# Kernel tuning notes

Measured on AMD Instinct MI355X. Metric: run time of the kernel, lower is better.

The kernel has to match this reference:

```python
import jax, jax.numpy as jnp
import numpy as np

H = 1024      # hidden_size
I = 512       # moe_intermediate_size
E = 8         # n_routed_experts
K = 2         # num_experts_per_tok
SI = I * 2    # shared expert intermediate (n_shared_experts=2)
B, S = 2, 1024


def setup_inputs() -> dict:
    key = jax.random.key(0)
    ks = jax.random.split(key, 9)
    s = 0.02
    return {
        "x": jax.random.normal(ks[0], (B, S, H), jnp.float32),
        "gate_w": jax.random.normal(ks[1], (E, H), jnp.float32) * s,
        "lb_bias": jnp.zeros((E,), jnp.float32),
        "expert_gate_w": jax.random.normal(ks[2], (E, I, H), jnp.float32) * s,
        "expert_up_w": jax.random.normal(ks[3], (E, I, H), jnp.float32) * s,
        "expert_down_w": jax.random.normal(ks[4], (E, H, I), jnp.float32) * s,
        "shared_gate_w": jax.random.normal(ks[5], (SI, H), jnp.float32) * s,
        "shared_up_w": jax.random.normal(ks[6], (SI, H), jnp.float32) * s,
        "shared_down_w": jax.random.normal(ks[7], (H, SI), jnp.float32) * s,
    }


def _mlp(x, gw, uw, dw):
    # SwiGLU: down( silu(gate(x)) * up(x) )
    return (jax.nn.silu(x @ gw.T) * (x @ uw.T)) @ dw.T


def reference(x, gate_w, lb_bias, expert_gate_w, expert_up_w, expert_down_w,
              shared_gate_w, shared_up_w, shared_down_w):
    b, s, h = x.shape
    xf = x.reshape(-1, h)                                   # [T, H]
    # --- SimpleRouter (sigmoid scoring) ---
    logits = xf @ gate_w.T + lb_bias                        # [T, E]
    scores = jax.nn.sigmoid(logits.astype(jnp.float32))
    topw, topi = jax.lax.top_k(scores, K)                   # [T, K]
    topw = (topw / (topw.sum(-1, keepdims=True) + 1e-8)).astype(x.dtype)
    # --- _process_local: per-expert dispatch/compute/combine ---
    # Faithful to torch source: expert_weights[mask].mean(dim=-1) collapses to a
    # SCALAR per expert (mean routing weight over all tokens sent to that expert).
    out = jnp.zeros_like(xf)
    for e in range(E):
        m = (topi == e)                                     # [T, K]
        sel = m.any(axis=-1)                                # [T]
        cnt = m.sum()
        wmean = (topw * m).sum() / jnp.maximum(cnt, 1).astype(topw.dtype)
        y = _mlp(xf, expert_gate_w[e], expert_up_w[e], expert_down_w[e])  # [T, H]
        out = out + jnp.where(sel[:, None], y * wmean, jnp.zeros((), x.dtype))
    out = out.reshape(b, s, h)
    # --- shared experts ---
    out = out + _mlp(x, shared_gate_w, shared_up_w, shared_down_w)
    return out
```

## Files before the change

### kernel.cpp

```cpp
#include <hip/hip_runtime.h>

#define H_DIM 1024
#define I_DIM 512
#define NE 8
#define SI_DIM 1024
#define NT 2048
#define NS 4096

typedef __bf16 bf16;
typedef __bf16 bf16x4 __attribute__((ext_vector_type(4)));
typedef __bf16 bf16x8 __attribute__((ext_vector_type(8)));
typedef float f32x4 __attribute__((ext_vector_type(4)));

#define W_EG 0
#define W_EU (NE * I_DIM * H_DIM)
#define W_ED (2 * NE * I_DIM * H_DIM)
#define W_SG (3 * NE * I_DIM * H_DIM)
#define W_SU (W_SG + SI_DIM * H_DIM)
#define W_SD (W_SU + SI_DIM * H_DIM)
#define W_TOT (W_SD + H_DIM * SI_DIM)

#define OFF_CNT 0
#define OFF_WM 64
#define OFF_BASE 128
#define OFF_TOPI 1024
#define OFF_TOPW (OFF_TOPI + NT * 8)
#define OFF_GSLOT (OFF_TOPW + NT * 8)
#define OFF_LISTS (OFF_GSLOT + NT * 8)
#define OFF_WB (OFF_LISTS + NS * 4)
#define OFF_XB (OFF_WB + W_TOT * 2)
#define OFF_XG (OFF_XB + NT * H_DIM * 2)
#define OFF_ACTE (OFF_XG + (NS + 128) * H_DIM * 2)
#define OFF_ACTS (OFF_ACTE + (NS + 128) * I_DIM * 2)
#define OFF_YDE (OFF_ACTS + (size_t)NT * SI_DIM * 2)
#define OFF_YDS (OFF_YDE + (size_t)NS * H_DIM * 2)

__device__ __forceinline__ bf16x4 cvt4(f32x4 v) {
  bf16x4 r;
  r.x = (bf16)v.x; r.y = (bf16)v.y; r.z = (bf16)v.z; r.w = (bf16)v.w;
  return r;
}

__device__ __forceinline__ void glds16(const bf16* g, bf16* l) {
  __builtin_amdgcn_global_load_lds(
      (const __attribute__((address_space(1))) unsigned int*)g,
      (__attribute__((address_space(3))) unsigned int*)l, 16, 0, 0);
}

__global__ __launch_bounds__(256) void convert_w(
    const float* __restrict__ eg, const float* __restrict__ eu,
    const float* __restrict__ ed, const float* __restrict__ sg,
    const float* __restrict__ su, const float* __restrict__ sd,
    bf16* __restrict__ wb) {
  size_t i = ((size_t)blockIdx.x * 256 + threadIdx.x) * 4;
  if (i >= W_TOT) return;
  const float* src;
  size_t o;
  if (i < W_EU)      { src = eg; o = i - W_EG; }
  else if (i < W_ED) { src = eu; o = i - W_EU; }
  else if (i < W_SG) { src = ed; o = i - W_ED; }
  else if (i < W_SU) { src = sg; o = i - W_SG; }
  else if (i < W_SD) { src = su; o = i - W_SU; }
  else               { src = sd; o = i - W_SD; }
  *(bf16x4*)(wb + i) = cvt4(*(const f32x4*)(src + o));
}

__global__ __launch_bounds__(256) void router_kernel(
    const float* __restrict__ x, const float* __restrict__ gw,
    const float* __restrict__ lb, int2* __restrict__ topi,
    float2* __restrict__ topw) {
  const int lane = threadIdx.x & 63;
  const int t = blockIdx.x * 4 + (threadIdx.x >> 6);
  const float* xr = x + (size_t)t * H_DIM;

  float s[NE];
#pragma unroll
  for (int e = 0; e < NE; e++) s[e] = 0.f;
#pragma unroll
  for (int k0 = 0; k0 < H_DIM; k0 += 256) {
    f32x4 xv = *(const f32x4*)(xr + k0 + lane * 4);
#pragma unroll
    for (int e = 0; e < NE; e++) {
      f32x4 gv = *(const f32x4*)(gw + e * H_DIM + k0 + lane * 4);
      s[e] += xv.x * gv.x + xv.y * gv.y + xv.z * gv.z + xv.w * gv.w;
    }
  }
#pragma unroll
  for (int e = 0; e < NE; e++) {
    float v = s[e];
#pragma unroll
    for (int off = 32; off > 0; off >>= 1) v += __shfl_xor(v, off);
    s[e] = v;
  }
  if (lane == 0) {
    float sc[NE];
#pragma unroll
    for (int e = 0; e < NE; e++) sc[e] = 1.f / (1.f + expf(-(s[e] + lb[e])));
    int i1 = 0;
#pragma unroll
    for (int e = 1; e < NE; e++)
      if (sc[e] > sc[i1]) i1 = e;
    int i2 = -1;
#pragma unroll
    for (int e = 0; e < NE; e++) {
      if (e == i1) continue;
      if (i2 < 0 || sc[e] > sc[i2]) i2 = e;
    }
    float w1 = sc[i1], w2 = sc[i2];
    float inv = 1.f / (w1 + w2 + 1e-8f);
    topi[t] = make_int2(i1, i2);
    topw[t] = make_float2(w1 * inv, w2 * inv);
  }
}

__global__ __launch_bounds__(512) void build_kernel(
    const int2* __restrict__ topi, const float2* __restrict__ topw,
    int* __restrict__ cnt, float* __restrict__ wm, int* __restrict__ base,
    int* __restrict__ lists, int2* __restrict__ gslot) {
  __shared__ int cnt_l[NE];
  __shared__ int base_l[NE + 1];
  const int e = threadIdx.x >> 6;
  const int lane = threadIdx.x & 63;

  int c = 0;
  float wacc = 0.f;
  for (int t0 = 0; t0 < NT; t0 += 64) {
    int2 ti = topi[t0 + lane];
    float2 tw = topw[t0 + lane];
    bool hit = (ti.x == e) || (ti.y == e);
    float w = (ti.x == e) ? tw.x : ((ti.y == e) ? tw.y : 0.f);
    c += __popcll(__ballot(hit));
#pragma unroll
    for (int off = 32; off > 0; off >>= 1) w += __shfl_xor(w, off);
    wacc += w;
  }
  if (lane == 0) {
    cnt_l[e] = c;
    cnt[e] = c;
    wm[e] = wacc / (float)(c > 0 ? c : 1);
  }
  __syncthreads();
  if (threadIdx.x == 0) {
    int b = 0;
    for (int i = 0; i < NE; i++) {
      base_l[i] = b;
      base[i] = b;
      b += cnt_l[i];
    }
    base_l[NE] = b;
    base[NE] = b;
  }
  __syncthreads();

  int pos = base_l[e];
  for (int t0 = 0; t0 < NT; t0 += 64) {
    int t = t0 + lane;
    int2 ti = topi[t];
    bool hit = (ti.x == e) || (ti.y == e);
    unsigned long long m = __ballot(hit);
    int pre = __popcll(m & ((1ull << lane) - 1ull));
    if (hit) {
      int g = pos + pre;
      lists[g] = t;
      if (ti.x == e) gslot[t].x = g;
      else gslot[t].y = g;
    }
    pos += __popcll(m);
  }
}

__global__ __launch_bounds__(256) void gather_kernel(
    const float* __restrict__ x, const int* __restrict__ lists,
    bf16* __restrict__ xg, bf16* __restrict__ xb) {
  int b = blockIdx.x;
  const float* src;
  bf16* dst;
  if (b < NS) {
    src = x + (size_t)lists[b] * H_DIM;
    dst = xg + (size_t)b * H_DIM;
  } else {
    int r = b - NS;
    src = x + (size_t)r * H_DIM;
    dst = xb + (size_t)r * H_DIM;
  }
  int c = threadIdx.x * 4;
  *(bf16x4*)(dst + c) = cvt4(*(const f32x4*)(src + c));
}

__global__ __launch_bounds__(256, 2) void gemm_gu(
    const bf16* __restrict__ wb, const bf16* __restrict__ xg,
    const bf16* __restrict__ xb, const int* __restrict__ cnt,
    const int* __restrict__ base, bf16* __restrict__ act_e,
    bf16* __restrict__ act_s) {
  const int z = blockIdx.z, colTile = blockIdx.x, rowTile = blockIdx.y;
  const bf16 *Ab, *Gb, *Ub;
  bf16* Cp;
  int ldc, mrem;
  if (z < NE) {
    if (colTile >= I_DIM / 128) return;
    int c = cnt[z];
    if (rowTile * 128 >= c) return;
    int rb = base[z] + rowTile * 128;
    Ab = xg + (size_t)rb * H_DIM;
    Gb = wb + W_EG + (size_t)z * I_DIM * H_DIM + (size_t)colTile * 128 * H_DIM;
    Ub = wb + W_EU + (size_t)z * I_DIM * H_DIM + (size_t)colTile * 128 * H_DIM;
    Cp = act_e + (size_t)rb * I_DIM + colTile * 128;
    ldc = I_DIM;
    mrem = c - rowTile * 128;
  } else {
    Ab = xb + (size_t)rowTile * 128 * H_DIM;
    Gb = wb + W_SG + (size_t)colTile * 128 * H_DIM;
    Ub = wb + W_SU + (size_t)colTile * 128 * H_DIM;
    Cp = act_s + (size_t)rowTile * 128 * SI_DIM + colTile * 128;
    ldc = SI_DIM;
    mrem = 128;
  }

  __shared__ __align__(16) bf16 As[128 * 64];
  __shared__ __align__(16) bf16 Bgs[128 * 64];
  __shared__ __align__(16) bf16 Bus[128 * 64];

  const int tid = threadIdx.x;
  const int lane = tid & 63, wave = tid >> 6;
  const int mw = (wave >> 1) * 64, nw = (wave & 1) * 64;
  const int l15 = lane & 15, quad = lane >> 4;
  const int srow = tid >> 3;
  const int scol = (tid & 7) * 8;

  f32x4 ag[4][4] = {};
  f32x4 au[4][4] = {};

  for (int k0 = 0; k0 < H_DIM; k0 += 64) {
#pragma unroll
    for (int r = 0; r < 4; r++) {
      int row = srow + r * 32;
      glds16(Ab + (size_t)row * H_DIM + k0 + scol, &As[row * 64 + scol]);
    }
#pragma unroll
    for (int r = 0; r < 4; r++) {
      int row = srow + r * 32;
      glds16(Gb + (size_t)row * H_DIM + k0 + scol, &Bgs[row * 64 + scol]);
    }
#pragma unroll
    for (int r = 0; r < 4; r++) {
      int row = srow + r * 32;
      glds16(Ub + (size_t)row * H_DIM + k0 + scol, &Bus[row * 64 + scol]);
    }
    __syncthreads();
#pragma unroll
    for (int kk = 0; kk < 2; kk++) {
      const int kof = kk * 32 + quad * 8;
      bf16x8 av[4], gv[4], uv[4];
#pragma unroll
      for (int i = 0; i < 4; i++) {
        av[i] = *(const bf16x8*)&As[(mw + i * 16 + l15) * 64 + kof];
        gv[i] = *(const bf16x8*)&Bgs[(nw + i * 16 + l15) * 64 + kof];
        uv[i] = *(const bf16x8*)&Bus[(nw + i * 16 + l15) * 64 + kof];
      }
#pragma unroll
      for (int i = 0; i < 4; i++)
#pragma unroll
        for (int j = 0; j < 4; j++) {
          ag[i][j] = __builtin_amdgcn_mfma_f32_16x16x32_bf16(av[i], gv[j], ag[i][j], 0, 0, 0);
          au[i][j] = __builtin_amdgcn_mfma_f32_16x16x32_bf16(av[i], uv[j], au[i][j], 0, 0, 0);
        }
    }
    __syncthreads();
  }

#pragma unroll
  for (int i = 0; i < 4; i++) {
#pragma unroll
    for (int rg = 0; rg < 4; rg++) {
      int rl = mw + i * 16 + quad * 4 + rg;
      if (rl < mrem) {
#pragma unroll
        for (int j = 0; j < 4; j++) {
          int c = nw + j * 16 + l15;
          float g = ag[i][j][rg], u = au[i][j][rg];
          Cp[(size_t)rl * ldc + c] = (bf16)((g / (1.f + __expf(-g))) * u);
        }
      }
    }
  }
}

__global__ __launch_bounds__(256, 2) void gemm_down(
    const bf16* __restrict__ wb, const bf16* __restrict__ act_e,
    const bf16* __restrict__ act_s, const int* __restrict__ cnt,
    const int* __restrict__ base, bf16* __restrict__ yd_e,
    bf16* __restrict__ yd_s) {
  const int z = blockIdx.z, colTile = blockIdx.x, rowTile = blockIdx.y;
  const bf16 *Ab, *Bb;
  bf16* Cp;
  int K, mrem;
  if (z < NE) {
    int c = cnt[z];
    if (rowTile * 128 >= c) return;
    int rb = base[z] + rowTile * 128;
    Ab = act_e + (size_t)rb * I_DIM;
    K = I_DIM;
    Bb = wb + W_ED + (size_t)z * H_DIM * I_DIM + (size_t)colTile * 128 * I_DIM;
    Cp = yd_e + (size_t)rb * H_DIM + colTile * 128;
    mrem = c - rowTile * 128;
  } else {
    Ab = act_s + (size_t)rowTile * 128 * SI_DIM;
    K = SI_DIM;
    Bb = wb + W_SD + (size_t)colTile * 128 * SI_DIM;
    Cp = yd_s + (size_t)rowTile * 128 * H_DIM + colTile * 128;
    mrem = 128;
  }

  __shared__ __align__(16) bf16 As[128 * 64];
  __shared__ __align__(16) bf16 Bs[128 * 64];

  const int tid = threadIdx.x;
  const int lane = tid & 63, wave = tid >> 6;
  const int mw = (wave >> 1) * 64, nw = (wave & 1) * 64;
  const int l15 = lane & 15, quad = lane >> 4;
  const int srow = tid >> 3;
  const int scol = (tid & 7) * 8;

  f32x4 acc[4][4] = {};

  for (int k0 = 0; k0 < K; k0 += 64) {
#pragma unroll
    for (int r = 0; r < 4; r++) {
      int row = srow + r * 32;
      glds16(Ab + (size_t)row * K + k0 + scol, &As[row * 64 + scol]);
    }
#pragma unroll
    for (int r = 0; r < 4; r++) {
      int row = srow + r * 32;
      glds16(Bb + (size_t)row * K + k0 + scol, &Bs[row * 64 + scol]);
    }
    __syncthreads();
#pragma unroll
    for (int kk = 0; kk < 2; kk++) {
      const int kof = kk * 32 + quad * 8;
      bf16x8 av[4], bv[4];
#pragma unroll
      for (int i = 0; i < 4; i++) {
        av[i] = *(const bf16x8*)&As[(mw + i * 16 + l15) * 64 + kof];
        bv[i] = *(const bf16x8*)&Bs[(nw + i * 16 + l15) * 64 + kof];
      }
#pragma unroll
      for (int i = 0; i < 4; i++)
#pragma unroll
        for (int j = 0; j < 4; j++)
          acc[i][j] = __builtin_amdgcn_mfma_f32_16x16x32_bf16(av[i], bv[j], acc[i][j], 0, 0, 0);
    }
    __syncthreads();
  }

#pragma unroll
  for (int i = 0; i < 4; i++) {
#pragma unroll
    for (int rg = 0; rg < 4; rg++) {
      int rl = mw + i * 16 + quad * 4 + rg;
      if (rl < mrem) {
#pragma unroll
        for (int j = 0; j < 4; j++) {
          int c = nw + j * 16 + l15;
          Cp[(size_t)rl * H_DIM + c] = (bf16)acc[i][j][rg];
        }
      }
    }
  }
}

__global__ __launch_bounds__(256) void combine_kernel(
    const bf16* __restrict__ yd_e, const bf16* __restrict__ yd_s,
    const int2* __restrict__ topi, const int2* __restrict__ gslot,
    const float* __restrict__ wm, float* __restrict__ out) {
  int t = blockIdx.x;
  int2 ei = topi[t];
  int2 gi = gslot[t];
  float w1 = wm[ei.x], w2 = wm[ei.y];
  int c = threadIdx.x * 4;
  bf16x4 y1 = *(const bf16x4*)(yd_e + (size_t)gi.x * H_DIM + c);
  bf16x4 y2 = *(const bf16x4*)(yd_e + (size_t)gi.y * H_DIM + c);
  bf16x4 ys = *(const bf16x4*)(yd_s + (size_t)t * H_DIM + c);
  f32x4 o;
  o.x = w1 * (float)y1.x + w2 * (float)y2.x + (float)ys.x;
  o.y = w1 * (float)y1.y + w2 * (float)y2.y + (float)ys.y;
  o.z = w1 * (float)y1.z + w2 * (float)y2.z + (float)ys.z;
  o.w = w1 * (float)y1.w + w2 * (float)y2.w + (float)ys.w;
  *(f32x4*)(out + (size_t)t * H_DIM + c) = o;
}

extern "C" void kernel_launch(void* const* d_in, const int* in_sizes, int n_in,
                              void* d_out, int out_size, void* d_ws,
                              size_t ws_size, hipStream_t stream) {
  (void)in_sizes; (void)n_in; (void)out_size; (void)ws_size;
  const float* x  = (const float*)d_in[0];
  const float* gw = (const float*)d_in[1];
  const float* lb = (const float*)d_in[2];
  const float* eg = (const float*)d_in[3];
  const float* eu = (const float*)d_in[4];
  const float* ed = (const float*)d_in[5];
  const float* sg = (const float*)d_in[6];
  const float* su = (const float*)d_in[7];
  const float* sd = (const float*)d_in[8];
  float* out = (float*)d_out;
  char* ws = (char*)d_ws;

  int* cnt     = (int*)(ws + OFF_CNT);
  float* wm    = (float*)(ws + OFF_WM);
  int* base    = (int*)(ws + OFF_BASE);
  int2* topi   = (int2*)(ws + OFF_TOPI);
  float2* topw = (float2*)(ws + OFF_TOPW);
  int2* gslot  = (int2*)(ws + OFF_GSLOT);
  int* lists   = (int*)(ws + OFF_LISTS);
  bf16* wb     = (bf16*)(ws + OFF_WB);
  bf16* xb     = (bf16*)(ws + OFF_XB);
  bf16* xg     = (bf16*)(ws + OFF_XG);
  bf16* act_e  = (bf16*)(ws + OFF_ACTE);
  bf16* act_s  = (bf16*)(ws + OFF_ACTS);
  bf16* yd_e   = (bf16*)(ws + OFF_YDE);
  bf16* yd_s   = (bf16*)(ws + OFF_YDS);

  convert_w<<<W_TOT / 1024, 256, 0, stream>>>(eg, eu, ed, sg, su, sd, wb);
  router_kernel<<<NT / 4, 256, 0, stream>>>(x, gw, lb, topi, topw);
  build_kernel<<<1, 512, 0, stream>>>(topi, topw, cnt, wm, base, lists, gslot);
  gather_kernel<<<NS + NT, 256, 0, stream>>>(x, lists, xg, xb);
  gemm_gu<<<dim3(8, 16, 9), 256, 0, stream>>>(wb, xg, xb, cnt, base, act_e, act_s);
  gemm_down<<<dim3(8, 16, 9), 256, 0, stream>>>(wb, act_e, act_s, cnt, base, yd_e, yd_s);
  combine_kernel<<<NT, 256, 0, stream>>>(yd_e, yd_s, topi, gslot, wm, out);
}
```

Before: 232.3 us.

## Fuse prep kernels, interleave gate/up weights, gather rows inside gate-up GEMM

Merges weight conversion, x conversion and routing into one prep kernel. The gate and up weights are interleaved in 16-row groups, so one GEMM tile computes gate and up columns together with a single B buffer. The separate gather kernel is dropped: gemm_gu reads token rows from the bf16 copy of x through a per-block row index list, so the xg buffer is never materialised. The grid doubles in x, and each block uses half the accumulators and less LDS, which may help occupancy, at the cost of indirect A loads.

```diff
diff --git a/kernel.cpp b/kernel.cpp
--- a/kernel.cpp
+++ b/kernel.cpp
@@ -12,13 +12,15 @@
 typedef __bf16 bf16x8 __attribute__((ext_vector_type(8)));
 typedef float f32x4 __attribute__((ext_vector_type(4)));
 
-#define W_EG 0
-#define W_EU (NE * I_DIM * H_DIM)
-#define W_ED (2 * NE * I_DIM * H_DIM)
-#define W_SG (3 * NE * I_DIM * H_DIM)
-#define W_SU (W_SG + SI_DIM * H_DIM)
-#define W_SD (W_SU + SI_DIM * H_DIM)
-#define W_TOT (W_SD + H_DIM * SI_DIM)
+#define W_GU 0
+#define W_DN 8388608ull
+#define W_SGU 12582912ull
+#define W_SDN 14680064ull
+#define W_TOT 15728640ull
+
+#define NWB 15360
+#define NXB 2048
+#define NRB 512
 
 #define OFF_CNT 0
 #define OFF_WM 64
@@ -29,9 +31,8 @@
 #define OFF_LISTS (OFF_GSLOT + NT * 8)
 #define OFF_WB (OFF_LISTS + NS * 4)
 #define OFF_XB (OFF_WB + W_TOT * 2)
-#define OFF_XG (OFF_XB + NT * H_DIM * 2)
-#define OFF_ACTE (OFF_XG + (NS + 128) * H_DIM * 2)
-#define OFF_ACTS (OFF_ACTE + (NS + 128) * I_DIM * 2)
+#define OFF_ACTE (OFF_XB + (size_t)NT * H_DIM * 2)
+#define OFF_ACTS (OFF_ACTE + (size_t)(NS + 128) * I_DIM * 2)
 #define OFF_YDE (OFF_ACTS + (size_t)NT * SI_DIM * 2)
 #define OFF_YDS (OFF_YDE + (size_t)NS * H_DIM * 2)
 
@@ -47,69 +48,83 @@
       (__attribute__((address_space(3))) unsigned int*)l, 16, 0, 0);
 }
 
-__global__ __launch_bounds__(256) void convert_w(
-    const float* __restrict__ eg, const float* __restrict__ eu,
-    const float* __restrict__ ed, const float* __restrict__ sg,
-    const float* __restrict__ su, const float* __restrict__ sd,
-    bf16* __restrict__ wb) {
-  size_t i = ((size_t)blockIdx.x * 256 + threadIdx.x) * 4;
-  if (i >= W_TOT) return;
-  const float* src;
-  size_t o;
-  if (i < W_EU)      { src = eg; o = i - W_EG; }
-  else if (i < W_ED) { src = eu; o = i - W_EU; }
-  else if (i < W_SG) { src = ed; o = i - W_ED; }
-  else if (i < W_SU) { src = sg; o = i - W_SG; }
-  else if (i < W_SD) { src = su; o = i - W_SU; }
-  else               { src = sd; o = i - W_SD; }
-  *(bf16x4*)(wb + i) = cvt4(*(const f32x4*)(src + o));
-}
-
-__global__ __launch_bounds__(256) void router_kernel(
+__global__ __launch_bounds__(256) void prep_kernel(
     const float* __restrict__ x, const float* __restrict__ gw,
-    const float* __restrict__ lb, int2* __restrict__ topi,
+    const float* __restrict__ lb, const float* __restrict__ eg,
+    const float* __restrict__ eu, const float* __restrict__ ed,
+    const float* __restrict__ sg, const float* __restrict__ su,
+    const float* __restrict__ sd, bf16* __restrict__ wb,
+    bf16* __restrict__ xb, int2* __restrict__ topi,
     float2* __restrict__ topw) {
-  const int lane = threadIdx.x & 63;
-  const int t = blockIdx.x * 4 + (threadIdx.x >> 6);
-  const float* xr = x + (size_t)t * H_DIM;
-
-  float s[NE];
-#pragma unroll
-  for (int e = 0; e < NE; e++) s[e] = 0.f;
-#pragma unroll
-  for (int k0 = 0; k0 < H_DIM; k0 += 256) {
-    f32x4 xv = *(const f32x4*)(xr + k0 + lane * 4);
+  const int bx = blockIdx.x;
+  const int tid = threadIdx.x;
+  if (bx < NWB) {
+    size_t i = ((size_t)bx * 256 + tid) * 4;
+    const float* src;
+    if (i < W_DN) {
+      size_t z = i >> 20;
+      int rem = (int)(i & ((1u << 20) - 1));
+      int rp = rem >> 10, k = rem & 1023;
+      int b = rp >> 4;
+      int sr = ((b >> 1) << 4) | (rp & 15);
+      src = ((b & 1) ? eu : eg) + (z << 19) + ((size_t)sr << 10) + k;
+    } else if (i < W_SGU) {
+      src = ed + (i - W_DN);
+    } else if (i < W_SDN) {
+      int rem = (int)(i - W_SGU);
+      int rp = rem >> 10, k = rem & 1023;
+      int b = rp >> 4;
+      int sr = ((b >> 1) << 4) | (rp & 15);
+      src = ((b & 1) ? su : sg) + ((size_t)sr << 10) + k;
+    } else {
+      src = sd + (i - W_SDN);
+    }
+    *(bf16x4*)(wb + i) = cvt4(*(const f32x4*)src);
+  } else if (bx < NWB + NXB) {
+    size_t i = ((size_t)(bx - NWB) * 256 + tid) * 4;
+    *(bf16x4*)(xb + i) = cvt4(*(const f32x4*)(x + i));
+  } else {
+    const int lane = tid & 63;
+    const int t = (bx - NWB - NXB) * 4 + (tid >> 6);
+    const float* xr = x + (size_t)t * H_DIM;
+    float s[NE];
+#pragma unroll
+    for (int e = 0; e < NE; e++) s[e] = 0.f;
+#pragma unroll
+    for (int k0 = 0; k0 < H_DIM; k0 += 256) {
+      f32x4 xv = *(const f32x4*)(xr + k0 + lane * 4);
+#pragma unroll
+      for (int e = 0; e < NE; e++) {
+        f32x4 gv = *(const f32x4*)(gw + e * H_DIM + k0 + lane * 4);
+        s[e] += xv.x * gv.x + xv.y * gv.y + xv.z * gv.z + xv.w * gv.w;
+      }
+    }
 #pragma unroll
     for (int e = 0; e < NE; e++) {
-      f32x4 gv = *(const f32x4*)(gw + e * H_DIM + k0 + lane * 4);
-      s[e] += xv.x * gv.x + xv.y * gv.y + xv.z * gv.z + xv.w * gv.w;
-    }
-  }
-#pragma unroll
-  for (int e = 0; e < NE; e++) {
-    float v = s[e];
-#pragma unroll
-    for (int off = 32; off > 0; off >>= 1) v += __shfl_xor(v, off);
-    s[e] = v;
-  }
-  if (lane == 0) {
-    float sc[NE];
-#pragma unroll
-    for (int e = 0; e < NE; e++) sc[e] = 1.f / (1.f + expf(-(s[e] + lb[e])));
-    int i1 = 0;
-#pragma unroll
-    for (int e = 1; e < NE; e++)
-      if (sc[e] > sc[i1]) i1 = e;
-    int i2 = -1;
-#pragma unroll
-    for (int e = 0; e < NE; e++) {
-      if (e == i1) continue;
-      if (i2 < 0 || sc[e] > sc[i2]) i2 = e;
-    }
-    float w1 = sc[i1], w2 = sc[i2];
-    float inv = 1.f / (w1 + w2 + 1e-8f);
-    topi[t] = make_int2(i1, i2);
-    topw[t] = make_float2(w1 * inv, w2 * inv);
+      float v = s[e];
+#pragma unroll
+      for (int off = 32; off > 0; off >>= 1) v += __shfl_xor(v, off);
+      s[e] = v;
+    }
+    if (lane == 0) {
+      float sc[NE];
+#pragma unroll
+      for (int e = 0; e < NE; e++) sc[e] = 1.f / (1.f + expf(-(s[e] + lb[e])));
+      int i1 = 0;
+#pragma unroll
+      for (int e = 1; e < NE; e++)
+        if (sc[e] > sc[i1]) i1 = e;
+      int i2 = -1;
+#pragma unroll
+      for (int e = 0; e < NE; e++) {
+        if (e == i1) continue;
+        if (i2 < 0 || sc[e] > sc[i2]) i2 = e;
+      }
+      float w1 = sc[i1], w2 = sc[i2];
+      float inv = 1.f / (w1 + w2 + 1e-8f);
+      topi[t] = make_int2(i1, i2);
+      topw[t] = make_float2(w1 * inv, w2 * inv);
+    }
   }
 }
 
@@ -147,7 +162,6 @@
       base[i] = b;
       b += cnt_l[i];
     }
-    base_l[NE] = b;
     base[NE] = b;
   }
   __syncthreads();
@@ -169,101 +183,74 @@
   }
 }
 
-__global__ __launch_bounds__(256) void gather_kernel(
-    const float* __restrict__ x, const int* __restrict__ lists,
-    bf16* __restrict__ xg, bf16* __restrict__ xb) {
-  int b = blockIdx.x;
-  const float* src;
-  bf16* dst;
-  if (b < NS) {
-    src = x + (size_t)lists[b] * H_DIM;
-    dst = xg + (size_t)b * H_DIM;
+__global__ __launch_bounds__(256, 2) void gemm_gu(
+    const bf16* __restrict__ wb, const bf16* __restrict__ xb,
+    const int* __restrict__ cnt, const int* __restrict__ base,
+    const int* __restrict__ lists, bf16* __restrict__ act_e,
+    bf16* __restrict__ act_s) {
+  const int z = blockIdx.z, ct = blockIdx.x, rt = blockIdx.y;
+  const bf16* Bb;
+  bf16* Cb;
+  int mrem, ldc;
+  __shared__ int rows_s[128];
+  __shared__ __align__(16) bf16 As[128 * 64];
+  __shared__ __align__(16) bf16 Bs[128 * 64];
+  const int tid = threadIdx.x;
+  if (z < NE) {
+    if (ct >= 8) return;
+    int c = cnt[z];
+    if (rt * 128 >= c) return;
+    int rb = base[z] + rt * 128;
+    mrem = c - rt * 128;
+    if (tid < 128) rows_s[tid] = lists[rb + (tid < mrem ? tid : mrem - 1)];
+    Bb = wb + W_GU + ((size_t)z << 20) + (size_t)ct * 128 * H_DIM;
+    Cb = act_e + (size_t)rb * I_DIM;
+    ldc = I_DIM;
   } else {
-    int r = b - NS;
-    src = x + (size_t)r * H_DIM;
-    dst = xb + (size_t)r * H_DIM;
-  }
-  int c = threadIdx.x * 4;
-  *(bf16x4*)(dst + c) = cvt4(*(const f32x4*)(src + c));
-}
-
-__global__ __launch_bounds__(256, 2) void gemm_gu(
-    const bf16* __restrict__ wb, const bf16* __restrict__ xg,
-    const bf16* __restrict__ xb, const int* __restrict__ cnt,
-    const int* __restrict__ base, bf16* __restrict__ act_e,
-    bf16* __restrict__ act_s) {
-  const int z = blockIdx.z, colTile = blockIdx.x, rowTile = blockIdx.y;
-  const bf16 *Ab, *Gb, *Ub;
-  bf16* Cp;
-  int ldc, mrem;
-  if (z < NE) {
-    if (colTile >= I_DIM / 128) return;
-    int c = cnt[z];
-    if (rowTile * 128 >= c) return;
-    int rb = base[z] + rowTile * 128;
-    Ab = xg + (size_t)rb * H_DIM;
-    Gb = wb + W_EG + (size_t)z * I_DIM * H_DIM + (size_t)colTile * 128 * H_DIM;
-    Ub = wb + W_EU + (size_t)z * I_DIM * H_DIM + (size_t)colTile * 128 * H_DIM;
-    Cp = act_e + (size_t)rb * I_DIM + colTile * 128;
-    ldc = I_DIM;
-    mrem = c - rowTile * 128;
-  } else {
-    Ab = xb + (size_t)rowTile * 128 * H_DIM;
-    Gb = wb + W_SG + (size_t)colTile * 128 * H_DIM;
-    Ub = wb + W_SU + (size_t)colTile * 128 * H_DIM;
-    Cp = act_s + (size_t)rowTile * 128 * SI_DIM + colTile * 128;
+    mrem = 128;
+    if (tid < 128) rows_s[tid] = rt * 128 + tid;
+    Bb = wb + W_SGU + (size_t)ct * 128 * H_DIM;
+    Cb = act_s + (size_t)rt * 128 * SI_DIM;
     ldc = SI_DIM;
-    mrem = 128;
-  }
-
-  __shared__ __align__(16) bf16 As[128 * 64];
-  __shared__ __align__(16) bf16 Bgs[128 * 64];
-  __shared__ __align__(16) bf16 Bus[128 * 64];
-
-  const int tid = threadIdx.x;
+  }
+  __syncthreads();
+
   const int lane = tid & 63, wave = tid >> 6;
   const int mw = (wave >> 1) * 64, nw = (wave & 1) * 64;
   const int l15 = lane & 15, quad = lane >> 4;
-  const int srow = tid >> 3;
-  const int scol = (tid & 7) * 8;
-
-  f32x4 ag[4][4] = {};
-  f32x4 au[4][4] = {};
-
+  const int srow = tid >> 3, scol = (tid & 7) * 8;
+
+  const bf16* ap[4];
+  const bf16* bp[4];
+#pragma unroll
+  for (int r = 0; r < 4; r++) {
+    ap[r] = xb + (size_t)rows_s[srow + r * 32] * H_DIM + scol;
+    bp[r] = Bb + (size_t)(srow + r * 32) * H_DIM + scol;
+  }
+
+  f32x4 acc[4][4] = {};
   for (int k0 = 0; k0 < H_DIM; k0 += 64) {
 #pragma unroll
-    for (int r = 0; r < 4; r++) {
-      int row = srow + r * 32;
-      glds16(Ab + (size_t)row * H_DIM + k0 + scol, &As[row * 64 + scol]);
-    }
-#pragma unroll
-    for (int r = 0; r < 4; r++) {
-      int row = srow + r * 32;
-      glds16(Gb + (size_t)row * H_DIM + k0 + scol, &Bgs[row * 64 + scol]);
-    }
-#pragma unroll
-    for (int r = 0; r < 4; r++) {
-      int row = srow + r * 32;
-      glds16(Ub + (size_t)row * H_DIM + k0 + scol, &Bus[row * 64 + scol]);
-    }
+    for (int r = 0; r < 4; r++)
+      glds16(ap[r] + k0, &As[(srow + r * 32) * 64 + scol]);
+#pragma unroll
+    for (int r = 0; r < 4; r++)
+      glds16(bp[r] + k0, &Bs[(srow + r * 32) * 64 + scol]);
     __syncthreads();
 #pragma unroll
     for (int kk = 0; kk < 2; kk++) {
       const int kof = kk * 32 + quad * 8;
-      bf16x8 av[4], gv[4], uv[4];
+      bf16x8 av[4], bv[4];
 #pragma unroll
       for (int i = 0; i < 4; i++) {
         av[i] = *(const bf16x8*)&As[(mw + i * 16 + l15) * 64 + kof];
-        gv[i] = *(const bf16x8*)&Bgs[(nw + i * 16 + l15) * 64 + kof];
-        uv[i] = *(const bf16x8*)&Bus[(nw + i * 16 + l15) * 64 + kof];
+        bv[i] = *(const bf16x8*)&Bs[(nw + i * 16 + l15) * 64 + kof];
       }
 #pragma unroll
       for (int i = 0; i < 4; i++)
 #pragma unroll
-        for (int j = 0; j < 4; j++) {
-          ag[i][j] = __builtin_amdgcn_mfma_f32_16x16x32_bf16(av[i], gv[j], ag[i][j], 0, 0, 0);
-          au[i][j] = __builtin_amdgcn_mfma_f32_16x16x32_bf16(av[i], uv[j], au[i][j], 0, 0, 0);
-        }
+        for (int j = 0; j < 4; j++)
+          acc[i][j] = __builtin_amdgcn_mfma_f32_16x16x32_bf16(av[i], bv[j], acc[i][j], 0, 0, 0);
     }
     __syncthreads();
   }
@@ -275,10 +262,11 @@
       int rl = mw + i * 16 + quad * 4 + rg;
       if (rl < mrem) {
 #pragma unroll
-        for (int j = 0; j < 4; j++) {
-          int c = nw + j * 16 + l15;
-          float g = ag[i][j][rg], u = au[i][j][rg];
-          Cp[(size_t)rl * ldc + c] = (bf16)((g / (1.f + __expf(-g))) * u);
+        for (int jp = 0; jp < 2; jp++) {
+          float g = acc[i][jp * 2][rg];
+          float u = acc[i][jp * 2 + 1][rg];
+          int c = ct * 64 + (nw >> 1) + jp * 16 + l15;
+          Cb[(size_t)rl * ldc + c] = (bf16)((g / (1.f + __expf(-g))) * u);
         }
       }
     }
@@ -290,25 +278,25 @@
     const bf16* __restrict__ act_s, const int* __restrict__ cnt,
     const int* __restrict__ base, bf16* __restrict__ yd_e,
     bf16* __restrict__ yd_s) {
-  const int z = blockIdx.z, colTile = blockIdx.x, rowTile = blockIdx.y;
+  const int z = blockIdx.z, ct = blockIdx.x, rt = blockIdx.y;
   const bf16 *Ab, *Bb;
-  bf16* Cp;
+  bf16* Cb;
   int K, mrem;
   if (z < NE) {
     int c = cnt[z];
-    if (rowTile * 128 >= c) return;
-    int rb = base[z] + rowTile * 128;
+    if (rt * 128 >= c) return;
+    int rb = base[z] + rt * 128;
+    mrem = c - rt * 128;
     Ab = act_e + (size_t)rb * I_DIM;
     K = I_DIM;
-    Bb = wb + W_ED + (size_t)z * H_DIM * I_DIM + (size_t)colTile * 128 * I_DIM;
-    Cp = yd_e + (size_t)rb * H_DIM + colTile * 128;
-    mrem = c - rowTile * 128;
+    Bb = wb + W_DN + ((size_t)z << 19) + (size_t)ct * 128 * I_DIM;
+    Cb = yd_e + (size_t)rb * H_DIM + ct * 128;
   } else {
-    Ab = act_s + (size_t)rowTile * 128 * SI_DIM;
+    mrem = 128;
+    Ab = act_s + (size_t)rt * 128 * SI_DIM;
     K = SI_DIM;
-    Bb = wb + W_SD + (size_t)colTile * 128 * SI_DIM;
-    Cp = yd_s + (size_t)rowTile * 128 * H_DIM + colTile * 128;
-    mrem = 128;
+    Bb = wb + W_SDN + (size_t)ct * 128 * SI_DIM;
+    Cb = yd_s + (size_t)rt * 128 * H_DIM + ct * 128;
   }
 
   __shared__ __align__(16) bf16 As[128 * 64];
@@ -318,22 +306,18 @@
   const int lane = tid & 63, wave = tid >> 6;
   const int mw = (wave >> 1) * 64, nw = (wave & 1) * 64;
   const int l15 = lane & 15, quad = lane >> 4;
-  const int srow = tid >> 3;
-  const int scol = (tid & 7) * 8;
+  const int srow = tid >> 3, scol = (tid & 7) * 8;
 
   f32x4 acc[4][4] = {};
-
   for (int k0 = 0; k0 < K; k0 += 64) {
 #pragma unroll
-    for (int r = 0; r < 4; r++) {
-      int row = srow + r * 32;
-      glds16(Ab + (size_t)row * K + k0 + scol, &As[row * 64 + scol]);
-    }
-#pragma unroll
-    for (int r = 0; r < 4; r++) {
-      int row = srow + r * 32;
-      glds16(Bb + (size_t)row * K + k0 + scol, &Bs[row * 64 + scol]);
-    }
+    for (int r = 0; r < 4; r++)
+      glds16(Ab + (size_t)(srow + r * 32) * K + k0 + scol,
+             &As[(srow + r * 32) * 64 + scol]);
+#pragma unroll
+    for (int r = 0; r < 4; r++)
+      glds16(Bb + (size_t)(srow + r * 32) * K + k0 + scol,
+             &Bs[(srow + r * 32) * 64 + scol]);
     __syncthreads();
 #pragma unroll
     for (int kk = 0; kk < 2; kk++) {
@@ -360,10 +344,8 @@
       int rl = mw + i * 16 + quad * 4 + rg;
       if (rl < mrem) {
 #pragma unroll
-        for (int j = 0; j < 4; j++) {
-          int c = nw + j * 16 + l15;
-          Cp[(size_t)rl * H_DIM + c] = (bf16)acc[i][j][rg];
-        }
+        for (int j = 0; j < 4; j++)
+          Cb[(size_t)rl * H_DIM + nw + j * 16 + l15] = (bf16)acc[i][j][rg];
       }
     }
   }
@@ -414,17 +396,17 @@
   int* lists   = (int*)(ws + OFF_LISTS);
   bf16* wb     = (bf16*)(ws + OFF_WB);
   bf16* xb     = (bf16*)(ws + OFF_XB);
-  bf16* xg     = (bf16*)(ws + OFF_XG);
   bf16* act_e  = (bf16*)(ws + OFF_ACTE);
   bf16* act_s  = (bf16*)(ws + OFF_ACTS);
   bf16* yd_e   = (bf16*)(ws + OFF_YDE);
   bf16* yd_s   = (bf16*)(ws + OFF_YDS);
 
-  convert_w<<<W_TOT / 1024, 256, 0, stream>>>(eg, eu, ed, sg, su, sd, wb);
-  router_kernel<<<NT / 4, 256, 0, stream>>>(x, gw, lb, topi, topw);
+  prep_kernel<<<NWB + NXB + NRB, 256, 0, stream>>>(x, gw, lb, eg, eu, ed, sg,
+                                                   su, sd, wb, xb, topi, topw);
   build_kernel<<<1, 512, 0, stream>>>(topi, topw, cnt, wm, base, lists, gslot);
-  gather_kernel<<<NS + NT, 256, 0, stream>>>(x, lists, xg, xb);
-  gemm_gu<<<dim3(8, 16, 9), 256, 0, stream>>>(wb, xg, xb, cnt, base, act_e, act_s);
-  gemm_down<<<dim3(8, 16, 9), 256, 0, stream>>>(wb, act_e, act_s, cnt, base, yd_e, yd_s);
+  gemm_gu<<<dim3(16, 16, 9), 256, 0, stream>>>(wb, xb, cnt, base, lists, act_e,
+                                               act_s);
+  gemm_down<<<dim3(8, 16, 9), 256, 0, stream>>>(wb, act_e, act_s, cnt, base,
+                                                yd_e, yd_s);
   combine_kernel<<<NT, 256, 0, stream>>>(yd_e, yd_s, topi, gslot, wm, out);
 }
```

Result: faster. 224.9 us (-3.2%).
